# Kernel tuning notes

Measured on AMD Instinct MI355X. Metric: run time of the kernel, lower is better.

The kernel has to match this reference:

```python
import jax, jax.numpy as jnp
import numpy as np

B, C, H, W = 8, 128, 128, 128
D_MODEL = C
D_INNER = 2 * D_MODEL          # expand=2 -> 256
D_STATE = 64
HEADDIM = 32                   # _resolve_headdim(128, 32) -> 32
NHEADS = D_INNER // HEADDIM    # 8
D_CONV = 4
CHUNK = 64
GN_GROUPS = 8                  # _group_count(128, 8)
D_XBC = D_INNER + 2 * D_STATE  # 384
D_INPROJ = 2 * D_INNER + 2 * D_STATE + NHEADS  # 648


def _group_norm(x, g, b, groups=GN_GROUPS, eps=1e-5):
    Bn, Cn, Hh, Ww = x.shape
    xr = x.reshape(Bn, groups, Cn // groups, Hh, Ww)
    mu = xr.mean(axis=(2, 3, 4), keepdims=True)
    var = xr.var(axis=(2, 3, 4), keepdims=True)
    xr = (xr - mu) * jax.lax.rsqrt(var + eps)
    return xr.reshape(Bn, Cn, Hh, Ww) * g[None, :, None, None] + b[None, :, None, None]


def _grid_sample_bilinear_border(img, grid):
    # img: (B,C,H,W); grid: (B,H,W,2) with (x,y) in [-1,1]; align_corners=True, border padding
    _, _, Hh, Ww = img.shape
    gx = jnp.clip((grid[..., 0] + 1.0) * 0.5 * (Ww - 1), 0.0, Ww - 1.0)
    gy = jnp.clip((grid[..., 1] + 1.0) * 0.5 * (Hh - 1), 0.0, Hh - 1.0)
    x0 = jnp.floor(gx); y0 = jnp.floor(gy)
    wx = gx - x0; wy = gy - y0
    x0i = x0.astype(jnp.int32); y0i = y0.astype(jnp.int32)
    x1i = jnp.minimum(x0i + 1, Ww - 1); y1i = jnp.minimum(y0i + 1, Hh - 1)
    def per_b(im, y0b, y1b, x0b, x1b, wxb, wyb):
        v00 = im[:, y0b, x0b]; v01 = im[:, y0b, x1b]
        v10 = im[:, y1b, x0b]; v11 = im[:, y1b, x1b]
        return (v00 * (1 - wxb) + v01 * wxb) * (1 - wyb) + (v10 * (1 - wxb) + v11 * wxb) * wyb
    return jax.vmap(per_b)(img, y0i, y1i, x0i, x1i, wx, wy)


def _mamba(seq, in_proj_w, conv_w, conv_b, dt_bias, A_log, D_skip, norm_g, out_w):
    # seq: (Bs, L, d_model) -> (Bs, L, d_model); Mamba2/SSD-style selective scan
    Bs, L, _ = seq.shape
    pad = (CHUNK - L % CHUNK) % CHUNK
    if pad:
        seq = jnp.pad(seq, ((0, 0), (0, pad), (0, 0)))
    Lp = L + pad
    zxbcdt = jnp.einsum('bld,ed->ble', seq, in_proj_w)
    z = zxbcdt[..., :D_INNER]
    xBC = zxbcdt[..., D_INNER:D_INNER + D_XBC]
    dt = jax.nn.softplus(zxbcdt[..., -NHEADS:] + dt_bias)  # (Bs,Lp,nh)
    # causal depthwise conv1d, kernel D_CONV
    xp = jnp.pad(xBC, ((0, 0), (D_CONV - 1, 0), (0, 0)))
    xBC = sum(conv_w[:, k] * xp[:, k:k + Lp, :] for k in range(D_CONV)) + conv_b
    xBC = jax.nn.silu(xBC)
    xs = xBC[..., :D_INNER].reshape(Bs, Lp, NHEADS, HEADDIM)
    Bm = xBC[..., D_INNER:D_INNER + D_STATE]
    Cm = xBC[..., D_INNER + D_STATE:]
    A = -jnp.exp(A_log)  # (nh,)
    def step(h, inp):
        x_t, B_t, C_t, dt_t = inp  # (Bs,nh,hd),(Bs,ds),(Bs,ds),(Bs,nh)
        dA = jnp.exp(dt_t * A)  # (Bs,nh)
        h = h * dA[..., None, None] + (dt_t[..., None] * x_t)[..., None] * B_t[:, None, None, :]
        y = jnp.einsum('bhds,bs->bhd', h, C_t)
        return h, y
    h0 = jnp.zeros((Bs, NHEADS, HEADDIM, D_STATE), seq.dtype)
    _, ys = jax.lax.scan(step, h0, (jnp.moveaxis(xs, 1, 0), jnp.moveaxis(Bm, 1, 0), jnp.moveaxis(Cm, 1, 0), jnp.moveaxis(dt, 1, 0)))
    ys = jnp.moveaxis(ys, 0, 1) + D_skip[None, None, :, None] * xs  # (Bs,Lp,nh,hd)
    y = ys.reshape(Bs, Lp, D_INNER) * jax.nn.silu(z)  # gated
    y = y * jax.lax.rsqrt(jnp.mean(y * y, axis=-1, keepdims=True) + 1e-5) * norm_g  # RMSNorm
    out = jnp.einsum('ble,de->bld', y, out_w)
    return out[:, :L] if pad else out


def _forward(x, dw_w, gn_g, gn_b, pw_w, pw_b, in_proj_w, conv_w, conv_b, dt_bias, A_log, D_skip, norm_g, out_w):
    Bn, Cn, Hh, Ww = x.shape
    dn = ('NCHW', 'OIHW', 'NCHW')
    # offset_net: depthwise 5x5 -> GroupNorm -> GELU -> 1x1
    h1 = jax.lax.conv_general_dilated(x, dw_w, (1, 1), 'SAME', feature_group_count=Cn, dimension_numbers=dn)
    h1 = jax.nn.gelu(_group_norm(h1, gn_g, gn_b), approximate=False)
    off = jax.lax.conv_general_dilated(h1, pw_w, (1, 1), 'SAME', dimension_numbers=dn) + pw_b[None, :, None, None]
    offset = jnp.tanh(off) * min(8.0, max(Hh, Ww) * 0.1)  # (B,1,H,W)
    gy = jnp.linspace(-1.0, 1.0, Hh, dtype=x.dtype)
    gx = jnp.linspace(-1.0, 1.0, Ww, dtype=x.dtype)
    base_y, base_x = jnp.meshgrid(gy, gx, indexing='ij')  # (H,W)
    off_n = offset[:, 0] * (2.0 / max(Hh - 1, 1))  # horizontal scan: vertical offsets
    grid = jnp.stack([jnp.broadcast_to(base_x, (Bn, Hh, Ww)), jnp.clip(base_y + off_n, -1.0, 1.0)], axis=-1)
    deformed = _grid_sample_bilinear_border(x, grid)
    seq = deformed.transpose(0, 2, 3, 1).reshape(Bn * Hh, Ww, Cn)  # (b h) w c
    out = _mamba(seq, in_proj_w, conv_w, conv_b, dt_bias, A_log, D_skip, norm_g, out_w)
    out_2d = out.reshape(Bn, Hh, Ww, Cn).transpose(0, 3, 1, 2)
    return out_2d, offset


def setup_inputs() -> dict:
    key = jax.random.key(0)
    ks = jax.random.split(key, 8)
    return {
        'x': jax.random.normal(ks[0], (B, C, H, W), jnp.float32),
        'dw_w': jax.random.normal(ks[1], (C, 1, 5, 5), jnp.float32) * 0.05,
        'gn_g': jnp.ones((C,), jnp.float32),
        'gn_b': jnp.zeros((C,), jnp.float32),
        'pw_w': jax.random.normal(ks[2], (1, C, 1, 1), jnp.float32) * 0.02,
        'pw_b': jnp.zeros((1,), jnp.float32),
        'in_proj_w': jax.random.normal(ks[3], (D_INPROJ, D_MODEL), jnp.float32) * 0.02,
        'conv_w': jax.random.normal(ks[4], (D_XBC, D_CONV), jnp.float32) * 0.1,
        'conv_b': jnp.zeros((D_XBC,), jnp.float32),
        'dt_bias': jax.random.normal(ks[5], (NHEADS,), jnp.float32) * 0.1,
        'A_log': jnp.log(jnp.arange(1, NHEADS + 1, dtype=jnp.float32)),
        'D_skip': jnp.ones((NHEADS,), jnp.float32),
        'norm_g': jnp.ones((D_INNER,), jnp.float32),
        'out_w': jax.random.normal(ks[6], (D_MODEL, D_INNER), jnp.float32) * 0.02,
    }


def reference(x, dw_w, gn_g, gn_b, pw_w, pw_b, in_proj_w, conv_w, conv_b, dt_bias, A_log, D_skip, norm_g, out_w):
    return _forward(x, dw_w, gn_g, gn_b, pw_w, pw_b, in_proj_w, conv_w, conv_b, dt_bias, A_log, D_skip, norm_g, out_w)
```

## Files before the change

### kernel.cpp

```cpp
#include <hip/hip_runtime.h>
#include <math.h>


typedef _Float16 half8 __attribute__((ext_vector_type(8)));
typedef _Float16 half4 __attribute__((ext_vector_type(4)));
typedef float f32x4 __attribute__((ext_vector_type(4)));

__device__ __forceinline__ float b2f(unsigned short u) {
  return __uint_as_float(((unsigned int)u) << 16);
}
__device__ __forceinline__ bool in_is_f32(const void* gng) {
  return ((const unsigned int*)gng)[0] == 0x3F800000u;
}

#define P_DWW 0
#define P_CW 3200
#define P_CB 4736
#define P_GNG 5120
#define P_GNB 5248
#define P_PWW 5376
#define P_PWB 5504
#define P_DTB 5505
#define P_ALOG 5513
#define P_DSKIP 5521
#define P_NG 5529

__global__ void k_prep_all(const void* dww, const void* cw, const void* cb,
                           const void* gng, const void* gnb, const void* pww,
                           const void* pwb, const void* dtbias, const void* alog,
                           const void* dskip, const void* ng,
                           const void* wproj, const void* outw,
                           float* __restrict__ P, float* __restrict__ gst,
                           _Float16* __restrict__ wprojh, _Float16* __restrict__ outwh) {
  bool f = in_is_f32(gng);
  int stride = gridDim.x * blockDim.x;
  for (int i = blockIdx.x * blockDim.x + threadIdx.x; i < 98304; i += stride) {
    int row = i >> 7;
    float v = 0.f;
    if (row < 648) v = f ? ((const float*)wproj)[i] : b2f(((const unsigned short*)wproj)[i]);
    wprojh[i] = (_Float16)v;
  }
  for (int i = blockIdx.x * blockDim.x + threadIdx.x; i < 32768; i += stride)
    outwh[i] = (_Float16)(f ? ((const float*)outw)[i] : b2f(((const unsigned short*)outw)[i]));
  if (blockIdx.x == 0) {
    int tid = threadIdx.x;
    if (tid < 128) gst[tid] = 0.f;
    auto cvt = [&](const void* src, int n, int off) {
      for (int i = tid; i < n; i += 256)
        P[off + i] = f ? ((const float*)src)[i] : b2f(((const unsigned short*)src)[i]);
    };
    cvt(dww, 3200, P_DWW);
    cvt(cw, 1536, P_CW);
    cvt(cb, 384, P_CB);
    cvt(gng, 128, P_GNG);
    cvt(gnb, 128, P_GNB);
    cvt(pww, 128, P_PWW);
    cvt(pwb, 1, P_PWB);
    cvt(dtbias, 8, P_DTB);
    cvt(alog, 8, P_ALOG);
    cvt(dskip, 8, P_DSKIP);
    cvt(ng, 256, P_NG);
  }
}

__global__ __launch_bounds__(256) void k_dwconv_v6(const void* __restrict__ x,
                                                   const void* __restrict__ gng,
                                                   const float* __restrict__ P,
                                                   _Float16* __restrict__ h1h,
                                                   float* __restrict__ gst) {
  int bc = blockIdx.x;
  int b = bc >> 7, c = bc & 127;
  bool f32x = in_is_f32(gng);
  __shared__ float red[8];
  const float* xf = (const float*)x + (size_t)bc * 16384;
  const unsigned short* xb = (const unsigned short*)x + (size_t)bc * 16384;
  float w[25];
#pragma unroll
  for (int k = 0; k < 25; ++k) w[k] = P[P_DWW + c * 25 + k];

  int ox = (threadIdx.x & 31) * 4;
  int y0 = (threadIdx.x >> 5) * 16;
  float win[5][12];

  auto loadrow = [&](int gy, float* d) {
#pragma unroll
    for (int k = 0; k < 12; ++k) d[k] = 0.f;
    if (gy >= 0 && gy < 128) {
      if (f32x) {
        const float* rp = xf + gy * 128;
        if (ox >= 4) {
          float4 v = *(const float4*)(rp + ox - 4);
          d[0] = v.x; d[1] = v.y; d[2] = v.z; d[3] = v.w;
        }
        float4 v0 = *(const float4*)(rp + ox);
        d[4] = v0.x; d[5] = v0.y; d[6] = v0.z; d[7] = v0.w;
        if (ox < 124) {
          float4 v1 = *(const float4*)(rp + ox + 4);
          d[8] = v1.x; d[9] = v1.y; d[10] = v1.z; d[11] = v1.w;
        }
      } else {
        const unsigned short* rp = xb + gy * 128;
        if (ox >= 4) {
          ushort4 u = *(const ushort4*)(rp + ox - 4);
          d[0] = b2f(u.x); d[1] = b2f(u.y); d[2] = b2f(u.z); d[3] = b2f(u.w);
        }
        ushort4 u0 = *(const ushort4*)(rp + ox);
        d[4] = b2f(u0.x); d[5] = b2f(u0.y); d[6] = b2f(u0.z); d[7] = b2f(u0.w);
        if (ox < 124) {
          ushort4 u1 = *(const ushort4*)(rp + ox + 4);
          d[8] = b2f(u1.x); d[9] = b2f(u1.y); d[10] = b2f(u1.z); d[11] = b2f(u1.w);
        }
      }
    }
  };

#pragma unroll
  for (int i = 0; i < 4; ++i) loadrow(y0 - 2 + i, win[i]);

  float s = 0.f, sq = 0.f;
  _Float16* hp = h1h + (size_t)bc * 16384;
#pragma unroll
  for (int yo = 0; yo < 16; ++yo) {
    loadrow(y0 + yo + 2, win[(yo + 4) % 5]);
    float o4[4] = {0.f, 0.f, 0.f, 0.f};
#pragma unroll
    for (int ky = 0; ky < 5; ++ky) {
      const float* r = win[(yo + ky) % 5];
#pragma unroll
      for (int j = 0; j < 4; ++j)
#pragma unroll
        for (int kx = 0; kx < 5; ++kx)
          o4[j] += w[ky * 5 + kx] * r[j + kx + 2];
    }
    half4 oh;
#pragma unroll
    for (int j = 0; j < 4; ++j) {
      oh[j] = (_Float16)o4[j];
      s += o4[j]; sq += o4[j] * o4[j];
    }
    *(half4*)&hp[(y0 + yo) * 128 + ox] = oh;
  }

  for (int o = 32; o; o >>= 1) { s += __shfl_down(s, o, 64); sq += __shfl_down(sq, o, 64); }
  int wv = threadIdx.x >> 6;
  if ((threadIdx.x & 63) == 0) { red[wv] = s; red[4 + wv] = sq; }
  __syncthreads();
  if (threadIdx.x == 0) {
    float ts = red[0] + red[1] + red[2] + red[3];
    float tq = red[4] + red[5] + red[6] + red[7];
    int g = (b << 3) + (c >> 4);
    atomicAdd(&gst[g * 2], ts);
    atomicAdd(&gst[g * 2 + 1], tq);
  }
}

__global__ __launch_bounds__(256) void k_gn_part(const _Float16* __restrict__ h1h,
                                                 const float* __restrict__ gst,
                                                 const float* __restrict__ P,
                                                 float* __restrict__ part) {
  int bh2 = blockIdx.x;
  int b = bh2 >> 8;
  int h = (bh2 & 255) >> 1;
  int half = bh2 & 1;
  int tid = threadIdx.x;
  int w = tid & 127;
  int sub = tid >> 7;
  __shared__ float ls[8];
  __shared__ float sacc[2][128];
  if (tid < 4) {
    const float invN = 1.f / 262144.f;
    int g = b * 8 + half * 4 + tid;
    float mean = gst[g * 2] * invN;
    float var = gst[g * 2 + 1] * invN - mean * mean;
    ls[tid * 2] = mean;
    ls[tid * 2 + 1] = rsqrtf(var + 1e-5f);
  }
  __syncthreads();
  int cbase = half * 64 + sub * 32;
  const _Float16* hb = h1h + (((size_t)(b * 128 + cbase)) * 128 + h) * 128 + w;
  float acc = 0.f;
#pragma unroll 4
  for (int ci = 0; ci < 32; ++ci) {
    int c = cbase + ci;
    float v = (float)hb[(size_t)ci * 16384];
    int lg = (sub * 32 + ci) >> 4;
    float nv = (v - ls[lg * 2]) * ls[lg * 2 + 1] * P[P_GNG + c] + P[P_GNB + c];
    float ge = 0.5f * nv * (1.f + erff(nv * 0.70710678118f));
    acc += ge * P[P_PWW + c];
  }
  sacc[sub][w] = acc;
  __syncthreads();
  if (sub == 0) part[(size_t)bh2 * 128 + w] = acc + sacc[1][w];
}

__global__ __launch_bounds__(256) void k_deform_v4(const void* __restrict__ x,
                                                   const void* __restrict__ gng,
                                                   const float* __restrict__ part,
                                                   const float* __restrict__ P,
                                                   _Float16* __restrict__ seqc,
                                                   float* __restrict__ dout,
                                                   int s0) {
  int bh = s0 + blockIdx.x;
  int b = bh >> 7, h = bh & 127;
  int tid = threadIdx.x;
  int w = tid & 127;
  int half = tid >> 7;
  bool f32x = in_is_f32(gng);
  __shared__ float t[128 * 129];
  float ofv = tanhf(part[(size_t)bh * 256 + w] + part[(size_t)bh * 256 + 128 + w] +
                    P[P_PWB]) * 8.0f;
  if (half == 0) dout[16777216 + bh * 128 + w] = ofv;
  float gy = -1.f + (2.f / 127.f) * (float)h + ofv * (2.f / 127.f);
  gy = fminf(fmaxf(gy, -1.f), 1.f);
  float py = (gy + 1.f) * 0.5f * 127.f;
  py = fminf(fmaxf(py, 0.f), 127.f);
  float y0f = floorf(py);
  float wy = py - y0f;
  int y0 = (int)y0f;
  int y1 = min(y0 + 1, 127);
  const float* xfb = (const float*)x + (size_t)b * 128 * 16384;
  const unsigned short* xbb = (const unsigned short*)x + (size_t)b * 128 * 16384;
  int c0 = half * 64;
  for (int i = 0; i < 64; ++i) {
    int c = c0 + i;
    size_t o0 = (size_t)c * 16384 + y0 * 128 + w;
    size_t o1 = (size_t)c * 16384 + y1 * 128 + w;
    float v0, v1;
    if (f32x) { v0 = xfb[o0]; v1 = xfb[o1]; }
    else      { v0 = b2f(xbb[o0]); v1 = b2f(xbb[o1]); }
    t[c * 129 + w] = v0 + wy * (v1 - v0);
  }
  __syncthreads();
  int c2 = tid & 127;
  int lb = (tid >> 7) * 64;
  _Float16* sp = seqc + (size_t)blockIdx.x * 16384;
  for (int i = 0; i < 64; ++i) {
    int l = lb + i;
    sp[l * 128 + c2] = (_Float16)t[c2 * 129 + l];
  }
}

__global__ __launch_bounds__(256) void k_gemm1_v6(const _Float16* __restrict__ seqh,
                                                  const _Float16* __restrict__ wprojh,
                                                  const float* __restrict__ P,
                                                  _Float16* __restrict__ zh,
                                                  _Float16* __restrict__ xch,
                                                  float* __restrict__ dtb) {
  __shared__ __align__(16) _Float16 lds[16384];
  _Float16* lA = lds;
  _Float16* lB = lds + 8192;
  int m0 = blockIdx.x * 128;
  int e0 = blockIdx.y * 128;
  int tid = threadIdx.x;
  int lane = tid & 63;
  int wv = tid >> 6;
  f32x4 acc[2][8];
#pragma unroll
  for (int rf = 0; rf < 2; ++rf)
#pragma unroll
    for (int cf = 0; cf < 8; ++cf) acc[rf][cf] = (f32x4){0.f, 0.f, 0.f, 0.f};

  int rsel = lane & 15, q = lane >> 4;
  for (int k0 = 0; k0 < 128; k0 += 64) {
    if (k0) __syncthreads();
#pragma unroll
    for (int p = 0; p < 4; ++p) {
      int idx = tid + 256 * p;
      int row = idx >> 3, ch = idx & 7;
      int dch = ch ^ (row & 7);
      *(half8*)&lA[row * 64 + dch * 8] =
          *(const half8*)&seqh[(size_t)(m0 + row) * 128 + k0 + ch * 8];
      *(half8*)&lB[row * 64 + dch * 8] =
          *(const half8*)&wprojh[(size_t)(e0 + row) * 128 + k0 + ch * 8];
    }
    __syncthreads();
#pragma unroll
    for (int kk = 0; kk < 2; ++kk) {
      half8 a[2];
#pragma unroll
      for (int rf = 0; rf < 2; ++rf) {
        int row = wv * 32 + rf * 16 + rsel;
        int ch = (kk * 4 + q) ^ (row & 7);
        a[rf] = *(const half8*)&lA[row * 64 + ch * 8];
      }
#pragma unroll
      for (int cf = 0; cf < 8; ++cf) {
        int row = cf * 16 + rsel;
        int ch = (kk * 4 + q) ^ (row & 7);
        half8 b = *(const half8*)&lB[row * 64 + ch * 8];
        acc[0][cf] = __builtin_amdgcn_mfma_f32_16x16x32_f16(a[0], b, acc[0][cf], 0, 0, 0);
        acc[1][cf] = __builtin_amdgcn_mfma_f32_16x16x32_f16(a[1], b, acc[1][cf], 0, 0, 0);
      }
    }
  }

  if (e0 < 256) {
#pragma unroll
    for (int rf = 0; rf < 2; ++rf) {
      int mb = m0 + wv * 32 + rf * 16 + q * 4;
#pragma unroll
      for (int cf = 0; cf < 8; ++cf) {
        _Float16* pz = zh + (size_t)mb * 256 + e0 + cf * 16 + rsel;
#pragma unroll
        for (int r = 0; r < 4; ++r) pz[(size_t)r * 256] = (_Float16)acc[rf][cf][r];
      }
    }
  } else if (e0 < 640) {
    __syncthreads();
#pragma unroll
    for (int rf = 0; rf < 2; ++rf) {
#pragma unroll
      for (int r = 0; r < 4; ++r) {
        int row = wv * 32 + rf * 16 + q * 4 + r;
#pragma unroll
        for (int cf = 0; cf < 8; ++cf)
          lds[row * 128 + cf * 16 + rsel] = (_Float16)acc[rf][cf][r];
      }
    }
    __syncthreads();
    int cc = tid & 127;
    int rh = tid >> 7;
    int eg = (e0 - 256) + cc;
    float w0 = P[P_CW + eg * 4 + 0], w1 = P[P_CW + eg * 4 + 1];
    float w2 = P[P_CW + eg * 4 + 2], w3 = P[P_CW + eg * 4 + 3];
    float bb = P[P_CB + eg];
    int r0 = rh * 64;
    float x0 = (r0 >= 3) ? (float)lds[(r0 - 3) * 128 + cc] : 0.f;
    float x1 = (r0 >= 2) ? (float)lds[(r0 - 2) * 128 + cc] : 0.f;
    float x2 = (r0 >= 1) ? (float)lds[(r0 - 1) * 128 + cc] : 0.f;
    _Float16* xo = xch + (size_t)m0 * 384 + eg;
    for (int r = r0; r < r0 + 64; ++r) {
      float x3 = (float)lds[r * 128 + cc];
      float a = bb + w0 * x0 + w1 * x1 + w2 * x2 + w3 * x3;
      xo[(size_t)r * 384] = (_Float16)(a / (1.f + __expf(-a)));
      x0 = x1; x1 = x2; x2 = x3;
    }
  } else {
#pragma unroll
    for (int rf = 0; rf < 2; ++rf) {
      int mb = m0 + wv * 32 + rf * 16 + q * 4;
      if (rsel < 8) {
        float bias = P[P_DTB + rsel];
#pragma unroll
        for (int r = 0; r < 4; ++r) {
          float dv = acc[rf][0][r] + bias;
          float sp = (dv > 20.f) ? dv : log1pf(__expf(dv));
          dtb[(size_t)(mb + r) * 8 + rsel] = sp;
        }
      }
    }
  }
}

__global__ __launch_bounds__(256) void k_ssd(const _Float16* __restrict__ xch,
                                             const float* __restrict__ dtb,
                                             const float* __restrict__ P,
                                             _Float16* __restrict__ ys) {
  int seq = blockIdx.x;
  int tid = threadIdx.x;
  int lane = tid & 63, wv = tid >> 6;
  int rsel = lane & 15, q = lane >> 4;
  __shared__ __align__(16) _Float16 G[128 * 128];
  __shared__ __align__(16) _Float16 Xt[32 * 128];
  __shared__ float dts[128 * 8];
  __shared__ float Ts[8 * 128];
  const _Float16* xb = xch + (size_t)seq * 49152;
  const float* dtp = dtb + (size_t)seq * 1024;

  for (int i = tid; i < 1024; i += 256) dts[i] = dtp[i];
  __syncthreads();
  if (tid < 8) {
    float a = 0.f;
    for (int l = 0; l < 128; ++l) { a += dts[l * 8 + tid]; Ts[tid * 128 + l] = a; }
  }

  f32x4 gacc[2][8];
#pragma unroll
  for (int rf = 0; rf < 2; ++rf)
#pragma unroll
    for (int cf = 0; cf < 8; ++cf) gacc[rf][cf] = (f32x4){0.f, 0.f, 0.f, 0.f};
#pragma unroll
  for (int kk = 0; kk < 2; ++kk) {
    half8 a[2];
#pragma unroll
    for (int rf = 0; rf < 2; ++rf) {
      int l = wv * 32 + rf * 16 + rsel;
      a[rf] = *(const half8*)&xb[(size_t)l * 384 + 320 + kk * 32 + q * 8];
    }
#pragma unroll
    for (int cf = 0; cf < 8; ++cf) {
      int j = cf * 16 + rsel;
      half8 b = *(const half8*)&xb[(size_t)j * 384 + 256 + kk * 32 + q * 8];
      gacc[0][cf] = __builtin_amdgcn_mfma_f32_16x16x32_f16(a[0], b, gacc[0][cf], 0, 0, 0);
      gacc[1][cf] = __builtin_amdgcn_mfma_f32_16x16x32_f16(a[1], b, gacc[1][cf], 0, 0, 0);
    }
  }
#pragma unroll
  for (int rf = 0; rf < 2; ++rf) {
#pragma unroll
    for (int r = 0; r < 4; ++r) {
      int l = wv * 32 + rf * 16 + q * 4 + r;
#pragma unroll
      for (int cf = 0; cf < 8; ++cf) {
        int j = cf * 16 + rsel;
        G[l * 128 + (((j >> 3) ^ (l & 7)) << 3) + (j & 7)] = (_Float16)gacc[rf][cf][r];
      }
    }
  }
  __syncthreads();

  _Float16* yp = ys + (size_t)seq * 32768;
  for (int h = 0; h < 8; ++h) {
    {
      int j = tid >> 1, ds = (tid & 1) * 16;
      float dtj = dts[j * 8 + h];
      half8 v0 = *(const half8*)&xb[(size_t)j * 384 + h * 32 + ds];
      half8 v1 = *(const half8*)&xb[(size_t)j * 384 + h * 32 + ds + 8];
#pragma unroll
      for (int e = 0; e < 8; ++e) {
        int d0 = ds + e, d1 = ds + 8 + e;
        Xt[d0 * 128 + (((j >> 3) ^ (d0 & 7)) << 3) + (j & 7)] = (_Float16)((float)v0[e] * dtj);
        Xt[d1 * 128 + (((j >> 3) ^ (d1 & 7)) << 3) + (j & 7)] = (_Float16)((float)v1[e] * dtj);
      }
    }
    __syncthreads();
    float Ah = -__expf(P[P_ALOG + h]);
    float Dk = P[P_DSKIP + h];
    f32x4 acc[2][2];
#pragma unroll
    for (int rf = 0; rf < 2; ++rf)
#pragma unroll
      for (int cf = 0; cf < 2; ++cf) acc[rf][cf] = (f32x4){0.f, 0.f, 0.f, 0.f};
#pragma unroll
    for (int kk = 0; kk < 4; ++kk) {
      int jb = kk * 32 + q * 8;
      int chk = kk * 4 + q;
      float4 tj0 = *(const float4*)&Ts[h * 128 + jb];
      float4 tj1 = *(const float4*)&Ts[h * 128 + jb + 4];
      float tj[8] = {tj0.x, tj0.y, tj0.z, tj0.w, tj1.x, tj1.y, tj1.z, tj1.w};
      half8 a[2];
#pragma unroll
      for (int rf = 0; rf < 2; ++rf) {
        int l = wv * 32 + rf * 16 + rsel;
        half8 g = *(const half8*)&G[l * 128 + ((chk ^ (l & 7)) << 3)];
        float Tl = Ts[h * 128 + l];
        half8 w;
#pragma unroll
        for (int e = 0; e < 8; ++e) {
          int j = jb + e;
          float m = (j <= l) ? __expf(Ah * (Tl - tj[e])) : 0.f;
          w[e] = (_Float16)((float)g[e] * m);
        }
        a[rf] = w;
      }
#pragma unroll
      for (int cf = 0; cf < 2; ++cf) {
        int d = cf * 16 + rsel;
        half8 b = *(const half8*)&Xt[d * 128 + ((chk ^ (d & 7)) << 3)];
        acc[0][cf] = __builtin_amdgcn_mfma_f32_16x16x32_f16(a[0], b, acc[0][cf], 0, 0, 0);
        acc[1][cf] = __builtin_amdgcn_mfma_f32_16x16x32_f16(a[1], b, acc[1][cf], 0, 0, 0);
      }
    }
#pragma unroll
    for (int rf = 0; rf < 2; ++rf) {
      int lb = wv * 32 + rf * 16 + q * 4;
#pragma unroll
      for (int cf = 0; cf < 2; ++cf) {
        int d = cf * 16 + rsel;
#pragma unroll
        for (int r = 0; r < 4; ++r) {
          int l = lb + r;
          float xv = (float)xb[(size_t)l * 384 + h * 32 + d];
          yp[(size_t)l * 256 + h * 32 + d] = (_Float16)(acc[rf][cf][r] + Dk * xv);
        }
      }
    }
    __syncthreads();
  }
}

__global__ __launch_bounds__(256) void k_gate_v8(const _Float16* __restrict__ ys,
                                                 const _Float16* __restrict__ zh,
                                                 const float* __restrict__ P,
                                                 _Float16* __restrict__ ynh) {
  int seq = blockIdx.x;
  size_t base = (size_t)seq * 32768;
  int lane = threadIdx.x & 63;
  int wv = threadIdx.x >> 6;
  int sub = lane >> 5;
  int ln = lane & 31;
  for (int it = 0; it < 16; ++it) {
    int l = it * 8 + wv * 2 + sub;
    size_t off = base + (size_t)l * 256 + ln * 8;
    half8 yv8 = *(const half8*)&ys[off];
    half8 zv8 = *(const half8*)&zh[off];
    float yg[8];
    float ss = 0.f;
#pragma unroll
    for (int e = 0; e < 8; ++e) {
      float zv = (float)zv8[e];
      float g = zv / (1.f + __expf(-zv));
      float y = (float)yv8[e] * g;
      yg[e] = y;
      ss += y * y;
    }
    ss += __shfl_xor(ss, 1, 64);
    ss += __shfl_xor(ss, 2, 64);
    ss += __shfl_xor(ss, 4, 64);
    ss += __shfl_xor(ss, 8, 64);
    ss += __shfl_xor(ss, 16, 64);
    float r = rsqrtf(ss * (1.f / 256.f) + 1e-5f);
    half8 o;
#pragma unroll
    for (int e = 0; e < 8; ++e) o[e] = (_Float16)(yg[e] * r * P[P_NG + ln * 8 + e]);
    *(half8*)&ynh[off] = o;
  }
}

__global__ __launch_bounds__(256) void k_gemm2_v3(const _Float16* __restrict__ ynh,
                                                  const _Float16* __restrict__ outwh,
                                                  float* __restrict__ dout,
                                                  int tok0) {
  __shared__ __align__(16) _Float16 lA[128 * 64];
  __shared__ __align__(16) _Float16 lB[64 * 64];
  int t0 = blockIdx.x * 64;
  int tid = threadIdx.x;
  int lane = tid & 63;
  int wv = tid >> 6;
  f32x4 acc[2][4];
#pragma unroll
  for (int rf = 0; rf < 2; ++rf)
#pragma unroll
    for (int cf = 0; cf < 4; ++cf) acc[rf][cf] = (f32x4){0.f, 0.f, 0.f, 0.f};

  int rsel = lane & 15, q = lane >> 4;
  for (int k0 = 0; k0 < 256; k0 += 64) {
    if (k0) __syncthreads();
#pragma unroll
    for (int p = 0; p < 4; ++p) {
      int idx = tid + 256 * p;
      int row = idx >> 3, ch = idx & 7;
      int dch = ch ^ (row & 7);
      *(half8*)&lA[row * 64 + dch * 8] =
          *(const half8*)&outwh[(size_t)row * 256 + k0 + ch * 8];
    }
#pragma unroll
    for (int p = 0; p < 2; ++p) {
      int idx = tid + 256 * p;
      int row = idx >> 3, ch = idx & 7;
      int dch = ch ^ (row & 7);
      *(half8*)&lB[row * 64 + dch * 8] =
          *(const half8*)&ynh[(size_t)(t0 + row) * 256 + k0 + ch * 8];
    }
    __syncthreads();
#pragma unroll
    for (int kk = 0; kk < 2; ++kk) {
      half8 a[2];
#pragma unroll
      for (int rf = 0; rf < 2; ++rf) {
        int row = wv * 32 + rf * 16 + rsel;
        int ch = (kk * 4 + q) ^ (row & 7);
        a[rf] = *(const half8*)&lA[row * 64 + ch * 8];
      }
#pragma unroll
      for (int cf = 0; cf < 4; ++cf) {
        int row = cf * 16 + rsel;
        int ch = (kk * 4 + q) ^ (row & 7);
        half8 b = *(const half8*)&lB[row * 64 + ch * 8];
        acc[0][cf] = __builtin_amdgcn_mfma_f32_16x16x32_f16(a[0], b, acc[0][cf], 0, 0, 0);
        acc[1][cf] = __builtin_amdgcn_mfma_f32_16x16x32_f16(a[1], b, acc[1][cf], 0, 0, 0);
      }
    }
  }

  int l0 = tok0 + t0;
  int b = l0 >> 14;
  int rem0 = l0 & 16383;
#pragma unroll
  for (int rf = 0; rf < 2; ++rf) {
    int cbase = wv * 32 + rf * 16 + q * 4;
#pragma unroll
    for (int cf = 0; cf < 4; ++cf) {
#pragma unroll
      for (int r = 0; r < 4; ++r) {
        dout[(size_t)(b * 128 + cbase + r) * 16384 + rem0 + cf * 16 + rsel] = acc[rf][cf][r];
      }
    }
  }
}

extern "C" void kernel_launch(void* const* d_in, const int* in_sizes, int n_in,
                              void* d_out, int out_size, void* d_ws, size_t ws_size,
                              hipStream_t stream) {
  const void* x      = d_in[0];
  const void* dww    = d_in[1];
  const void* gng    = d_in[2];
  const void* gnb    = d_in[3];
  const void* pww    = d_in[4];
  const void* pwb    = d_in[5];
  const void* wproj  = d_in[6];
  const void* cw     = d_in[7];
  const void* cb     = d_in[8];
  const void* dtbias = d_in[9];
  const void* alog   = d_in[10];
  const void* dskip  = d_in[11];
  const void* ng     = d_in[12];
  const void* outw   = d_in[13];
  float* out = (float*)d_out;

  char* ws = (char*)d_ws;
  float* gst        = (float*)(ws + 0);
  float* P          = (float*)(ws + 8192);
  _Float16* wprojh  = (_Float16*)(ws + 40960);
  _Float16* outwh   = (_Float16*)(ws + 372736);
  float* part       = (float*)(ws + 503808);
  char* cbase       = ws + 1552384;

  _Float16* h1h = (_Float16*)out;

  const int opts[11] = {1024, 512, 256, 128, 64, 32, 16, 8, 4, 2, 1};
  int CH = 1;
  for (int i = 0; i < 11; ++i) {
    if (1552384ull + (unsigned long long)opts[i] * 266240ull <= (unsigned long long)ws_size) {
      CH = opts[i];
      break;
    }
  }
  int NC = 1024 / CH;

  _Float16* seqh = (_Float16*)(cbase);
  _Float16* zh   = (_Float16*)(cbase + (size_t)CH * 32768);
  _Float16* xch  = (_Float16*)(cbase + (size_t)CH * 98304);
  float* dtbf    = (float*)(cbase + (size_t)CH * 196608);
  _Float16* ysh  = (_Float16*)(cbase + (size_t)CH * 200704);
  _Float16* ynh  = xch;

  k_prep_all<<<128, 256, 0, stream>>>(dww, cw, cb, gng, gnb, pww, pwb, dtbias,
                                      alog, dskip, ng, wproj, outw, P, gst,
                                      wprojh, outwh);
  k_dwconv_v6<<<1024, 256, 0, stream>>>(x, gng, P, h1h, gst);
  k_gn_part<<<2048, 256, 0, stream>>>(h1h, gst, P, part);

  int M = CH * 128;
  for (int c = 0; c < NC; ++c) {
    int s0 = c * CH;
    k_deform_v4<<<CH, 256, 0, stream>>>(x, gng, part, P, seqh, out, s0);
    k_gemm1_v6<<<dim3(M / 128, 6), 256, 0, stream>>>(seqh, wprojh, P, zh, xch, dtbf);
    k_ssd<<<CH, 256, 0, stream>>>(xch, dtbf, P, ysh);
    k_gate_v8<<<CH, 256, 0, stream>>>(ysh, zh, P, ynh);
    k_gemm2_v3<<<dim3(M / 64), 256, 0, stream>>>(ynh, outwh, out, s0 * 128);
  }
}
```

Measured before the change: 494.2 us.

## Fuse SiLU gating and RMSNorm into SSD and output GEMM, removing gate kernel

The separate gate kernel is removed. The SSD kernel now applies the SiLU(z) gate, accumulates per-token sums of squares, and writes a per-token rsqrt scale. The output GEMM multiplies the staged activations by that scale, and the norm gain is folded into the fp16 out-projection weights during prep. The aim is to save one full read and write of the gated activations and one launch per chunk. The change also pads the conv LDS stride to 132 to reduce bank conflicts and unrolls the deform gather by two. In exchange the SSD epilogue does more work and an extra gather of z.

```diff
diff --git a/kernel.cpp b/kernel.cpp
--- a/kernel.cpp
+++ b/kernel.cpp
@@ -40,8 +40,12 @@
     if (row < 648) v = f ? ((const float*)wproj)[i] : b2f(((const unsigned short*)wproj)[i]);
     wprojh[i] = (_Float16)v;
   }
-  for (int i = blockIdx.x * blockDim.x + threadIdx.x; i < 32768; i += stride)
-    outwh[i] = (_Float16)(f ? ((const float*)outw)[i] : b2f(((const unsigned short*)outw)[i]));
+  for (int i = blockIdx.x * blockDim.x + threadIdx.x; i < 32768; i += stride) {
+    int e = i & 255;
+    float wv = f ? ((const float*)outw)[i] : b2f(((const unsigned short*)outw)[i]);
+    float ngv = f ? ((const float*)ng)[e] : b2f(((const unsigned short*)ng)[e]);
+    outwh[i] = (_Float16)(wv * ngv);
+  }
   if (blockIdx.x == 0) {
     int tid = threadIdx.x;
     if (tid < 128) gst[tid] = 0.f;
@@ -193,7 +197,7 @@
   if (sub == 0) part[(size_t)bh2 * 128 + w] = acc + sacc[1][w];
 }
 
-__global__ __launch_bounds__(256) void k_deform_v4(const void* __restrict__ x,
+__global__ __launch_bounds__(256) void k_deform_v5(const void* __restrict__ x,
                                                    const void* __restrict__ gng,
                                                    const float* __restrict__ part,
                                                    const float* __restrict__ P,
@@ -221,14 +225,18 @@
   const float* xfb = (const float*)x + (size_t)b * 128 * 16384;
   const unsigned short* xbb = (const unsigned short*)x + (size_t)b * 128 * 16384;
   int c0 = half * 64;
-  for (int i = 0; i < 64; ++i) {
-    int c = c0 + i;
-    size_t o0 = (size_t)c * 16384 + y0 * 128 + w;
-    size_t o1 = (size_t)c * 16384 + y1 * 128 + w;
-    float v0, v1;
-    if (f32x) { v0 = xfb[o0]; v1 = xfb[o1]; }
-    else      { v0 = b2f(xbb[o0]); v1 = b2f(xbb[o1]); }
-    t[c * 129 + w] = v0 + wy * (v1 - v0);
+  for (int i = 0; i < 64; i += 2) {
+    int ca = c0 + i, cb2 = c0 + i + 1;
+    size_t a0 = (size_t)ca * 16384 + y0 * 128 + w;
+    size_t a1 = (size_t)ca * 16384 + y1 * 128 + w;
+    size_t b0 = (size_t)cb2 * 16384 + y0 * 128 + w;
+    size_t b1 = (size_t)cb2 * 16384 + y1 * 128 + w;
+    float va0, va1, vb0, vb1;
+    if (f32x) { va0 = xfb[a0]; va1 = xfb[a1]; vb0 = xfb[b0]; vb1 = xfb[b1]; }
+    else      { va0 = b2f(xbb[a0]); va1 = b2f(xbb[a1]);
+                vb0 = b2f(xbb[b0]); vb1 = b2f(xbb[b1]); }
+    t[ca * 129 + w] = va0 + wy * (va1 - va0);
+    t[cb2 * 129 + w] = vb0 + wy * (vb1 - vb0);
   }
   __syncthreads();
   int c2 = tid & 127;
@@ -240,13 +248,13 @@
   }
 }
 
-__global__ __launch_bounds__(256) void k_gemm1_v6(const _Float16* __restrict__ seqh,
+__global__ __launch_bounds__(256) void k_gemm1_v7(const _Float16* __restrict__ seqh,
                                                   const _Float16* __restrict__ wprojh,
                                                   const float* __restrict__ P,
                                                   _Float16* __restrict__ zh,
                                                   _Float16* __restrict__ xch,
                                                   float* __restrict__ dtb) {
-  __shared__ __align__(16) _Float16 lds[16384];
+  __shared__ __align__(16) _Float16 lds[16896];
   _Float16* lA = lds;
   _Float16* lB = lds + 8192;
   int m0 = blockIdx.x * 128;
@@ -314,7 +322,7 @@
         int row = wv * 32 + rf * 16 + q * 4 + r;
 #pragma unroll
         for (int cf = 0; cf < 8; ++cf)
-          lds[row * 128 + cf * 16 + rsel] = (_Float16)acc[rf][cf][r];
+          lds[row * 132 + cf * 16 + rsel] = (_Float16)acc[rf][cf][r];
       }
     }
     __syncthreads();
@@ -325,12 +333,12 @@
     float w2 = P[P_CW + eg * 4 + 2], w3 = P[P_CW + eg * 4 + 3];
     float bb = P[P_CB + eg];
     int r0 = rh * 64;
-    float x0 = (r0 >= 3) ? (float)lds[(r0 - 3) * 128 + cc] : 0.f;
-    float x1 = (r0 >= 2) ? (float)lds[(r0 - 2) * 128 + cc] : 0.f;
-    float x2 = (r0 >= 1) ? (float)lds[(r0 - 1) * 128 + cc] : 0.f;
+    float x0 = (r0 >= 3) ? (float)lds[(r0 - 3) * 132 + cc] : 0.f;
+    float x1 = (r0 >= 2) ? (float)lds[(r0 - 2) * 132 + cc] : 0.f;
+    float x2 = (r0 >= 1) ? (float)lds[(r0 - 1) * 132 + cc] : 0.f;
     _Float16* xo = xch + (size_t)m0 * 384 + eg;
     for (int r = r0; r < r0 + 64; ++r) {
-      float x3 = (float)lds[r * 128 + cc];
+      float x3 = (float)lds[r * 132 + cc];
       float a = bb + w0 * x0 + w1 * x1 + w2 * x2 + w3 * x3;
       xo[(size_t)r * 384] = (_Float16)(a / (1.f + __expf(-a)));
       x0 = x1; x1 = x2; x2 = x3;
@@ -352,10 +360,12 @@
   }
 }
 
-__global__ __launch_bounds__(256) void k_ssd(const _Float16* __restrict__ xch,
-                                             const float* __restrict__ dtb,
-                                             const float* __restrict__ P,
-                                             _Float16* __restrict__ ys) {
+__global__ __launch_bounds__(256) void k_ssd_v2(const _Float16* __restrict__ xch,
+                                                const _Float16* __restrict__ zh,
+                                                const float* __restrict__ dtb,
+                                                const float* __restrict__ P,
+                                                _Float16* __restrict__ ys,
+                                                float* __restrict__ rr) {
   int seq = blockIdx.x;
   int tid = threadIdx.x;
   int lane = tid & 63, wv = tid >> 6;
@@ -365,6 +375,7 @@
   __shared__ float dts[128 * 8];
   __shared__ float Ts[8 * 128];
   const _Float16* xb = xch + (size_t)seq * 49152;
+  const _Float16* zb = zh + (size_t)seq * 32768;
   const float* dtp = dtb + (size_t)seq * 1024;
 
   for (int i = tid; i < 1024; i += 256) dts[i] = dtp[i];
@@ -408,6 +419,12 @@
     }
   }
   __syncthreads();
+
+  float ssq[2][4];
+#pragma unroll
+  for (int rf = 0; rf < 2; ++rf)
+#pragma unroll
+    for (int r = 0; r < 4; ++r) ssq[rf][r] = 0.f;
 
   _Float16* yp = ys + (size_t)seq * 32768;
   for (int h = 0; h < 8; ++h) {
@@ -471,53 +488,34 @@
         for (int r = 0; r < 4; ++r) {
           int l = lb + r;
           float xv = (float)xb[(size_t)l * 384 + h * 32 + d];
-          yp[(size_t)l * 256 + h * 32 + d] = (_Float16)(acc[rf][cf][r] + Dk * xv);
+          float zv = (float)zb[(size_t)l * 256 + h * 32 + d];
+          float y = acc[rf][cf][r] + Dk * xv;
+          float yg = y * (zv / (1.f + __expf(-zv)));
+          ssq[rf][r] += yg * yg;
+          yp[(size_t)l * 256 + h * 32 + d] = (_Float16)yg;
         }
       }
     }
     __syncthreads();
   }
-}
-
-__global__ __launch_bounds__(256) void k_gate_v8(const _Float16* __restrict__ ys,
-                                                 const _Float16* __restrict__ zh,
-                                                 const float* __restrict__ P,
-                                                 _Float16* __restrict__ ynh) {
-  int seq = blockIdx.x;
-  size_t base = (size_t)seq * 32768;
-  int lane = threadIdx.x & 63;
-  int wv = threadIdx.x >> 6;
-  int sub = lane >> 5;
-  int ln = lane & 31;
-  for (int it = 0; it < 16; ++it) {
-    int l = it * 8 + wv * 2 + sub;
-    size_t off = base + (size_t)l * 256 + ln * 8;
-    half8 yv8 = *(const half8*)&ys[off];
-    half8 zv8 = *(const half8*)&zh[off];
-    float yg[8];
-    float ss = 0.f;
-#pragma unroll
-    for (int e = 0; e < 8; ++e) {
-      float zv = (float)zv8[e];
-      float g = zv / (1.f + __expf(-zv));
-      float y = (float)yv8[e] * g;
-      yg[e] = y;
-      ss += y * y;
-    }
-    ss += __shfl_xor(ss, 1, 64);
-    ss += __shfl_xor(ss, 2, 64);
-    ss += __shfl_xor(ss, 4, 64);
-    ss += __shfl_xor(ss, 8, 64);
-    ss += __shfl_xor(ss, 16, 64);
-    float r = rsqrtf(ss * (1.f / 256.f) + 1e-5f);
-    half8 o;
-#pragma unroll
-    for (int e = 0; e < 8; ++e) o[e] = (_Float16)(yg[e] * r * P[P_NG + ln * 8 + e]);
-    *(half8*)&ynh[off] = o;
-  }
-}
-
-__global__ __launch_bounds__(256) void k_gemm2_v3(const _Float16* __restrict__ ynh,
+
+  float* rp = rr + (size_t)seq * 128;
+#pragma unroll
+  for (int rf = 0; rf < 2; ++rf) {
+#pragma unroll
+    for (int r = 0; r < 4; ++r) {
+      float ss = ssq[rf][r];
+      ss += __shfl_xor(ss, 1, 64);
+      ss += __shfl_xor(ss, 2, 64);
+      ss += __shfl_xor(ss, 4, 64);
+      ss += __shfl_xor(ss, 8, 64);
+      if (rsel == 0) rp[wv * 32 + rf * 16 + q * 4 + r] = rsqrtf(ss * (1.f / 256.f) + 1e-5f);
+    }
+  }
+}
+
+__global__ __launch_bounds__(256) void k_gemm2_v4(const _Float16* __restrict__ ysg,
+                                                  const float* __restrict__ rr,
                                                   const _Float16* __restrict__ outwh,
                                                   float* __restrict__ dout,
                                                   int tok0) {
@@ -549,8 +547,12 @@
       int idx = tid + 256 * p;
       int row = idx >> 3, ch = idx & 7;
       int dch = ch ^ (row & 7);
-      *(half8*)&lB[row * 64 + dch * 8] =
-          *(const half8*)&ynh[(size_t)(t0 + row) * 256 + k0 + ch * 8];
+      float rv = rr[t0 + row];
+      half8 v = *(const half8*)&ysg[(size_t)(t0 + row) * 256 + k0 + ch * 8];
+      half8 o;
+#pragma unroll
+      for (int e = 0; e < 8; ++e) o[e] = (_Float16)((float)v[e] * rv);
+      *(half8*)&lB[row * 64 + dch * 8] = o;
     }
     __syncthreads();
 #pragma unroll
@@ -621,7 +623,7 @@
   const int opts[11] = {1024, 512, 256, 128, 64, 32, 16, 8, 4, 2, 1};
   int CH = 1;
   for (int i = 0; i < 11; ++i) {
-    if (1552384ull + (unsigned long long)opts[i] * 266240ull <= (unsigned long long)ws_size) {
+    if (1552384ull + (unsigned long long)opts[i] * 266752ull <= (unsigned long long)ws_size) {
       CH = opts[i];
       break;
     }
@@ -633,7 +635,7 @@
   _Float16* xch  = (_Float16*)(cbase + (size_t)CH * 98304);
   float* dtbf    = (float*)(cbase + (size_t)CH * 196608);
   _Float16* ysh  = (_Float16*)(cbase + (size_t)CH * 200704);
-  _Float16* ynh  = xch;
+  float* rrf     = (float*)(cbase + (size_t)CH * 266240);
 
   k_prep_all<<<128, 256, 0, stream>>>(dww, cw, cb, gng, gnb, pww, pwb, dtbias,
                                       alog, dskip, ng, wproj, outw, P, gst,
@@ -644,10 +646,9 @@
   int M = CH * 128;
   for (int c = 0; c < NC; ++c) {
     int s0 = c * CH;
-    k_deform_v4<<<CH, 256, 0, stream>>>(x, gng, part, P, seqh, out, s0);
-    k_gemm1_v6<<<dim3(M / 128, 6), 256, 0, stream>>>(seqh, wprojh, P, zh, xch, dtbf);
-    k_ssd<<<CH, 256, 0, stream>>>(xch, dtbf, P, ysh);
-    k_gate_v8<<<CH, 256, 0, stream>>>(ysh, zh, P, ynh);
-    k_gemm2_v3<<<dim3(M / 64), 256, 0, stream>>>(ynh, outwh, out, s0 * 128);
-  }
-}
+    k_deform_v5<<<CH, 256, 0, stream>>>(x, gng, part, P, seqh, out, s0);
+    k_gemm1_v7<<<dim3(M / 128, 6), 256, 0, stream>>>(seqh, wprojh, P, zh, xch, dtbf);
+    k_ssd_v2<<<CH, 256, 0, stream>>>(xch, zh, dtbf, P, ysh, rrf);
+    k_gemm2_v4<<<dim3(M / 64), 256, 0, stream>>>(ysh, rrf, outwh, out, s0 * 128);
+  }
+}
```

After: 469.1 us. 1.05x faster.
